# Performance work log

Measured on AMD Instinct MI355X. Metric: run time of the kernel, lower is better.

Reference implementation:

```python
import jax, jax.numpy as jnp
import numpy as np

D_MODEL, D_STATE, D_CONV, EXPAND = 1024, 16, 4, 2
D_INNER = EXPAND * D_MODEL          # 2048
DT_RANK = D_MODEL // 16             # 64
B, L = 2, 1024


def setup_inputs() -> dict:
    key = jax.random.key(0)
    ks = jax.random.split(key, 10)
    x = jax.random.normal(ks[0], (B, L, D_MODEL), dtype=jnp.float32)
    ln_w = jnp.ones((D_MODEL,), jnp.float32)
    ln_b = jnp.zeros((D_MODEL,), jnp.float32)
    in_proj_w = jax.random.normal(ks[1], (2 * D_INNER, D_MODEL), jnp.float32) * (D_MODEL ** -0.5)
    conv_w = jax.random.normal(ks[2], (D_INNER, 1, D_CONV), jnp.float32) * (D_CONV ** -0.5)
    conv_b = jnp.zeros((D_INNER,), jnp.float32)
    x_proj_w = jax.random.normal(ks[3], (DT_RANK + 2 * D_STATE, D_INNER), jnp.float32) * (D_INNER ** -0.5)
    dt_proj_w = jax.random.normal(ks[4], (D_INNER, DT_RANK), jnp.float32) * (DT_RANK ** -0.5)
    # dt bias: inverse-softplus of dt sampled log-uniform in [1e-3, 1e-1] (mamba init)
    dt = jnp.exp(jax.random.uniform(ks[5], (D_INNER,)) * (np.log(0.1) - np.log(1e-3)) + np.log(1e-3))
    dt_proj_b = dt + jnp.log(-jnp.expm1(-dt))
    # A_log: log of [1..d_state] repeated per channel (S4D-real init)
    A_log = jnp.log(jnp.broadcast_to(jnp.arange(1, D_STATE + 1, dtype=jnp.float32), (D_INNER, D_STATE)))
    D = jnp.ones((D_INNER,), jnp.float32)
    out_proj_w = jax.random.normal(ks[6], (D_MODEL, D_INNER), jnp.float32) * (D_INNER ** -0.5)
    return dict(x=x, ln_w=ln_w, ln_b=ln_b, in_proj_w=in_proj_w, conv_w=conv_w,
                conv_b=conv_b, x_proj_w=x_proj_w, dt_proj_w=dt_proj_w,
                dt_proj_b=dt_proj_b, A_log=A_log, D=D, out_proj_w=out_proj_w)


def _layernorm(x, w, b, eps=1e-5):
    mu = jnp.mean(x, axis=-1, keepdims=True)
    var = jnp.mean(jnp.square(x - mu), axis=-1, keepdims=True)
    return (x - mu) * jax.lax.rsqrt(var + eps) * w + b


def _mamba(h, in_proj_w, conv_w, conv_b, x_proj_w, dt_proj_w, dt_proj_b, A_log, D, out_proj_w):
    # h: (B, L, d_model)
    xz = jnp.einsum('bld,ed->ble', h, in_proj_w)          # (B,L,2*d_inner)
    x_in, z = jnp.split(xz, 2, axis=-1)                   # each (B,L,d_inner)
    # depthwise causal conv1d
    kernel = jnp.transpose(conv_w, (2, 1, 0))             # (d_conv, 1, d_inner) LIO
    x_conv = jax.lax.conv_general_dilated(
        x_in, kernel, window_strides=(1,), padding=[(D_CONV - 1, 0)],
        dimension_numbers=('NLC', 'LIO', 'NLC'), feature_group_count=D_INNER)
    x_conv = jax.nn.silu(x_conv + conv_b)                 # (B,L,d_inner)
    # input-dependent SSM parameters
    x_dbl = jnp.einsum('bld,ed->ble', x_conv, x_proj_w)   # (B,L,dt_rank+2*d_state)
    dt, B_ssm, C_ssm = jnp.split(x_dbl, [DT_RANK, DT_RANK + D_STATE], axis=-1)
    dt = jax.nn.softplus(jnp.einsum('blr,dr->bld', dt, dt_proj_w) + dt_proj_b)  # (B,L,d_inner)
    A = -jnp.exp(A_log)                                   # (d_inner, d_state)
    deltaA = jnp.exp(dt[..., None] * A)                   # (B,L,d_inner,d_state)
    deltaBu = dt[..., None] * B_ssm[:, :, None, :] * x_conv[..., None]
    # selective scan: h_t = deltaA_t * h_{t-1} + deltaBu_t (parallel associative scan over L)
    def combine(left, right):
        a_l, b_l = left
        a_r, b_r = right
        return a_l * a_r, b_l * a_r + b_r
    _, states = jax.lax.associative_scan(combine, (deltaA, deltaBu), axis=1)
    y = jnp.einsum('blds,bls->bld', states, C_ssm) + x_conv * D
    y = y * jax.nn.silu(z)
    return jnp.einsum('bld,ed->ble', y, out_proj_w)       # (B,L,d_model)


def reference(x, ln_w, ln_b, in_proj_w, conv_w, conv_b, x_proj_w, dt_proj_w,
              dt_proj_b, A_log, D, out_proj_w):
    h = _layernorm(x, ln_w, ln_b)
    return x + _mamba(h, in_proj_w, conv_w, conv_b, x_proj_w, dt_proj_w,
                      dt_proj_b, A_log, D, out_proj_w)
```

## Files before the change

kernel.cpp:

```cpp
#include <hip/hip_runtime.h>
#include <hip/hip_bf16.h>
#include <math.h>

#define DM   1024
#define DI   2048
#define DS   16
#define DTR  64
#define NB   2
#define LL   1024
#define MR   (NB*LL)
#define XDBL 96
#define NC   32
#define CL   32

typedef _Float16 half8  __attribute__((ext_vector_type(8)));
typedef _Float16 half4v __attribute__((ext_vector_type(4)));
typedef float    floatx4 __attribute__((ext_vector_type(4)));

__device__ __forceinline__ void gload_lds16(const void* g, void* l) {
  __builtin_amdgcn_global_load_lds(
      (const __attribute__((address_space(1))) void*)g,
      (__attribute__((address_space(3))) void*)l, 16, 0, 0);
}

__global__ __launch_bounds__(256) void front_kernel(
    const float* __restrict__ x, const float* __restrict__ ln_w,
    const float* __restrict__ ln_b,
    const float* __restrict__ w_in, const float* __restrict__ w_out,
    const float* __restrict__ w_xp, const float* __restrict__ w_dt,
    _Float16* __restrict__ h_h,
    _Float16* __restrict__ w_in_h, _Float16* __restrict__ w_out_h,
    _Float16* __restrict__ w_xp_h, _Float16* __restrict__ w_dt_h) {
  const int blk = blockIdx.x;
  if (blk < MR) {
    __shared__ float sA[4], sB[4];
    const float* xr = x + (size_t)blk * DM;
    float s = 0.f, ss = 0.f;
    for (int i = threadIdx.x; i < DM; i += 256) {
      float v = xr[i];
      s += v; ss += v * v;
    }
    for (int o = 32; o > 0; o >>= 1) {
      s  += __shfl_down(s, o, 64);
      ss += __shfl_down(ss, o, 64);
    }
    const int wid = threadIdx.x >> 6, lid = threadIdx.x & 63;
    if (lid == 0) { sA[wid] = s; sB[wid] = ss; }
    __syncthreads();
    if (threadIdx.x == 0) {
      float S = sA[0] + sA[1] + sA[2] + sA[3];
      float SS = sB[0] + sB[1] + sB[2] + sB[3];
      float mu = S / DM;
      sA[0] = mu;
      sB[0] = rsqrtf(SS / DM - mu * mu + 1e-5f);
    }
    __syncthreads();
    const float mu = sA[0], rs = sB[0];
    for (int i = threadIdx.x; i < DM; i += 256)
      h_h[(size_t)blk * DM + i] = (_Float16)((xr[i] - mu) * rs * ln_w[i] + ln_b[i]);
    return;
  }
  int i = (blk - MR) * 256 + threadIdx.x;
  const int N0 = 1048576, N1 = 524288, N2 = 49152, N3 = 32768;
  const float* s; _Float16* d; int off;
  if (i < N0)            { s = w_in;  d = w_in_h;  off = i; }
  else if (i < N0+N1)    { s = w_out; d = w_out_h; off = i - N0; }
  else if (i < N0+N1+N2) { s = w_xp;  d = w_xp_h;  off = i - N0 - N1; }
  else if (i < N0+N1+N2+N3) { s = w_dt; d = w_dt_h; off = i - N0 - N1 - N2; }
  else return;
  float4 v = ((const float4*)s)[off];
  half4v h = {(_Float16)v.x, (_Float16)v.y, (_Float16)v.z, (_Float16)v.w};
  ((half4v*)d)[off] = h;
}

template <int EPI, int TN>
__global__ __launch_bounds__(256) void gemm_mfma(
    const _Float16* __restrict__ A,
    const _Float16* __restrict__ W,
    void* __restrict__ Cv, void* __restrict__ C2v,
    const float* __restrict__ extra, int ldc,
    int M, int N, int K, int kchunk) {
  constexpr int NT = TN / 32;
  constexpr int WSLOT = TN / 16;
  __shared__ alignas(16) _Float16 As[2][128 * 32];
  __shared__ alignas(16) _Float16 Ws[2][TN * 32];
  const int t = threadIdx.x;
  const int wave = t >> 6, lane = t & 63;
  const int m0 = blockIdx.y * 128, n0 = blockIdx.x * TN;
  const int k_beg = blockIdx.z * kchunk;
  const int nk = kchunk >> 5;
  const int wm = (wave >> 1) * 64, wn = (wave & 1) * (TN / 2);
  floatx4 acc[4][NT];
#pragma unroll
  for (int i = 0; i < 4; i++)
#pragma unroll
    for (int j = 0; j < NT; j++) acc[i][j] = {0.f, 0.f, 0.f, 0.f};

  const int fr = lane & 15;
  const int kc8 = lane >> 4;

  auto stage = [&](int buf, int k0) {
    for (int sl = wave; sl < 8; sl += 4) {
      const int idx = sl * 64 + lane;
      const int row = idx >> 2, kc = idx & 3;
      gload_lds16(A + (size_t)(m0 + row) * K + k0 + kc * 8, &As[buf][sl * 512]);
    }
    for (int sl = wave; sl < WSLOT; sl += 4) {
      const int idx = sl * 64 + lane;
      const int row = idx >> 2, kc = idx & 3;
      const int wrow = (n0 + row < N) ? row : 0;
      gload_lds16(W + (size_t)(n0 + wrow) * K + k0 + kc * 8, &Ws[buf][sl * 512]);
    }
  };

  stage(0, k_beg);
  int cur = 0;
  for (int ki = 0; ki < nk; ki++) {
    __syncthreads();
    if (ki + 1 < nk) stage(cur ^ 1, k_beg + ((ki + 1) << 5));
    half8 af[4], wf[NT];
#pragma unroll
    for (int i = 0; i < 4; i++)
      af[i] = *(const half8*)&As[cur][(wm + i * 16 + fr) * 32 + kc8 * 8];
#pragma unroll
    for (int j = 0; j < NT; j++)
      wf[j] = *(const half8*)&Ws[cur][(wn + j * 16 + fr) * 32 + kc8 * 8];
#pragma unroll
    for (int i = 0; i < 4; i++)
#pragma unroll
      for (int j = 0; j < NT; j++)
        acc[i][j] = __builtin_amdgcn_mfma_f32_16x16x32_f16(af[i], wf[j], acc[i][j], 0, 0, 0);
    cur ^= 1;
  }

  const int col = lane & 15, rowq = lane >> 4;
#pragma unroll
  for (int i = 0; i < 4; i++) {
#pragma unroll
    for (int j = 0; j < NT; j++) {
      const int n = n0 + wn + j * 16 + col;
      if (n < N) {
#pragma unroll
        for (int r = 0; r < 4; r++) {
          const int m = m0 + wm + i * 16 + rowq * 4 + r;
          float v = acc[i][j][r];
          if (EPI == 0) {
            if (n < DI) ((_Float16*)Cv )[(size_t)m * DI + n]      = (_Float16)v;
            else        ((_Float16*)C2v)[(size_t)m * DI + n - DI] = (_Float16)v;
          } else if (EPI == 1) {
            v += extra[n];
            v = (v > 20.f) ? v : log1pf(expf(v));
            ((float*)Cv)[(size_t)m * ldc + n] = v;
          } else if (EPI == 4) {
            ((float*)Cv)[((size_t)blockIdx.z * M + m) * ldc + n] = v;
          }
        }
      }
    }
  }
}

__global__ __launch_bounds__(256) void xproj_reduce(
    const float* __restrict__ part,
    float* __restrict__ x_dbl, _Float16* __restrict__ dtr) {
  const int idx = blockIdx.x * 256 + threadIdx.x;
  const int m = idx / XDBL, c = idx - m * XDBL;
  float s = 0.f;
#pragma unroll
  for (int z = 0; z < 16; z++) s += part[(size_t)z * (MR * XDBL) + idx];
  x_dbl[idx] = s;
  if (c < DTR) dtr[m * DTR + c] = (_Float16)s;
}

__global__ __launch_bounds__(256) void out_reduce(
    const float* __restrict__ x, const float* __restrict__ part,
    float* __restrict__ out) {
  const int i = blockIdx.x * 256 + threadIdx.x;
  float4 a  = ((const float4*)x)[i];
  float4 p0 = ((const float4*)part)[i];
  float4 p1 = ((const float4*)(part + (size_t)MR * DM))[i];
  float4 r = make_float4(a.x + p0.x + p1.x, a.y + p0.y + p1.y,
                         a.z + p0.z + p1.z, a.w + p0.w + p1.w);
  ((float4*)out)[i] = r;
}

__global__ __launch_bounds__(256) void conv_silu_kernel(
    const _Float16* __restrict__ xin, const float* __restrict__ cw,
    const float* __restrict__ cb, _Float16* __restrict__ xc) {
  const int idx = blockIdx.x * 256 + threadIdx.x;
  const int d8 = idx & (DI / 8 - 1);
  const int ml = idx >> 8;
  const int l  = ml & (LL - 1);
  const int d0 = d8 * 8;
  half8 xr[4];
  const half8 zero = {0, 0, 0, 0, 0, 0, 0, 0};
#pragma unroll
  for (int k = 0; k < 4; k++) {
    const int lp = l - 3 + k;
    xr[k] = (lp >= 0) ? *(const half8*)&xin[(size_t)(ml - 3 + k) * DI + d0] : zero;
  }
  half8 o;
#pragma unroll
  for (int j = 0; j < 8; j++) {
    float acc = cb[d0 + j];
#pragma unroll
    for (int k = 0; k < 4; k++)
      acc += (float)xr[k][j] * cw[(d0 + j) * 4 + k];
    o[j] = (_Float16)(acc / (1.f + __expf(-acc)));
  }
  *(half8*)&xc[(size_t)ml * DI + d0] = o;
}

__device__ __forceinline__ bool load_a(const float* __restrict__ A_log, int d,
                                       float* a) {
  const float4* Ap = (const float4*)(A_log + (size_t)d * DS);
  bool fast = true;
#pragma unroll
  for (int i = 0; i < 4; i++) {
    float4 v = Ap[i];
    a[4 * i + 0] = -__expf(v.x); a[4 * i + 1] = -__expf(v.y);
    a[4 * i + 2] = -__expf(v.z); a[4 * i + 3] = -__expf(v.w);
  }
#pragma unroll
  for (int s = 0; s < DS; s++)
    fast = fast && (fabsf(a[s] + (float)(s + 1)) < 1e-4f);
  return fast;
}

__global__ __launch_bounds__(256) void scan_phase1(
    const _Float16* __restrict__ xc,
    const float* __restrict__ xdbl,
    const float* __restrict__ dtm,
    const float* __restrict__ A_log,
    float* __restrict__ HE,
    float* __restrict__ SA) {
  __shared__ float Bs[CL][DS];
  const int bi = blockIdx.x;
  const int dblk = bi & 7;
  const int c = (bi >> 3) & (NC - 1);
  const int b = bi >> 8;
  const int t = threadIdx.x;
  const int d = dblk * 256 + t;
  const int mlbase = b * LL + c * CL;

  for (int i = t; i < CL * DS; i += 256) {
    int tt = i >> 4, s = i & 15;
    Bs[tt][s] = xdbl[(size_t)(mlbase + tt) * XDBL + DTR + s];
  }

  float a[DS];
  const bool fast = load_a(A_log, d, a);
  float h[DS];
#pragma unroll
  for (int s = 0; s < DS; s++) h[s] = 0.f;
  float S = 0.f;
  __syncthreads();

  if (fast) {
    for (int tt = 0; tt < CL; tt++) {
      const size_t ml = mlbase + tt;
      const float dtv = dtm[ml * DI + d];
      const float u   = (float)xc[ml * DI + d];
      const float du  = dtv * u;
      S += dtv;
      const float r = __expf(-dtv);
      float P = 1.f;
#pragma unroll
      for (int s = 0; s < DS; s++) {
        P *= r;
        h[s] = P * h[s] + du * Bs[tt][s];
      }
    }
  } else {
    for (int tt = 0; tt < CL; tt++) {
      const size_t ml = mlbase + tt;
      const float dtv = dtm[ml * DI + d];
      const float u   = (float)xc[ml * DI + d];
      const float du  = dtv * u;
      S += dtv;
#pragma unroll
      for (int s = 0; s < DS; s++)
        h[s] = __expf(dtv * a[s]) * h[s] + du * Bs[tt][s];
    }
  }
  const size_t base = ((size_t)(b * NC + c) * DS) * DI + d;
#pragma unroll
  for (int s = 0; s < DS; s++) HE[base + (size_t)s * DI] = h[s];
  SA[(size_t)(b * NC + c) * DI + d] = S;
}

__global__ __launch_bounds__(256) void scan_phase2(
    const float* __restrict__ A_log,
    const float* __restrict__ SA,
    float* __restrict__ HE) {
  const int idx = blockIdx.x * 256 + threadIdx.x;
  const int d = idx & (DI - 1);
  const int s = (idx >> 11) & (DS - 1);
  const int b = idx >> 15;
  const float a = -__expf(A_log[(size_t)d * DS + s]);
  float Hc = 0.f;
  for (int c = 0; c < NC; c++) {
    const size_t o = ((size_t)(b * NC + c) * DS + s) * DI + d;
    const float he = HE[o];
    const float P = __expf(a * SA[(size_t)(b * NC + c) * DI + d]);
    HE[o] = Hc;
    Hc = P * Hc + he;
  }
}

__global__ __launch_bounds__(256) void scan_phase3(
    const _Float16* __restrict__ xc,
    const float* __restrict__ xdbl,
    const float* __restrict__ dtm,
    const _Float16* __restrict__ zbuf,
    const float* __restrict__ A_log,
    const float* __restrict__ Dvec,
    const float* __restrict__ HE,
    _Float16* __restrict__ y) {
  __shared__ float Bs[CL][DS];
  __shared__ float Cs[CL][DS];
  const int bi = blockIdx.x;
  const int dblk = bi & 7;
  const int c = (bi >> 3) & (NC - 1);
  const int b = bi >> 8;
  const int t = threadIdx.x;
  const int d = dblk * 256 + t;
  const int mlbase = b * LL + c * CL;

  for (int i = t; i < CL * DS; i += 256) {
    int tt = i >> 4, s = i & 15;
    const size_t ro = (size_t)(mlbase + tt) * XDBL + DTR + s;
    Bs[tt][s] = xdbl[ro];
    Cs[tt][s] = xdbl[ro + DS];
  }

  float a[DS];
  const bool fast = load_a(A_log, d, a);
  float h[DS];
  const size_t base = ((size_t)(b * NC + c) * DS) * DI + d;
#pragma unroll
  for (int s = 0; s < DS; s++) h[s] = HE[base + (size_t)s * DI];
  const float Dv = Dvec[d];
  __syncthreads();

  if (fast) {
    for (int tt = 0; tt < CL; tt++) {
      const size_t ml = mlbase + tt;
      const float dtv = dtm[ml * DI + d];
      const float u   = (float)xc[ml * DI + d];
      const float du  = dtv * u;
      const float r = __expf(-dtv);
      float P = 1.f, p = 0.f;
#pragma unroll
      for (int s = 0; s < DS; s++) {
        P *= r;
        h[s] = P * h[s] + du * Bs[tt][s];
        p += h[s] * Cs[tt][s];
      }
      const float zv = (float)zbuf[ml * DI + d];
      const float sil = zv / (1.f + __expf(-zv));
      y[ml * DI + d] = (_Float16)((p + u * Dv) * sil);
    }
  } else {
    for (int tt = 0; tt < CL; tt++) {
      const size_t ml = mlbase + tt;
      const float dtv = dtm[ml * DI + d];
      const float u   = (float)xc[ml * DI + d];
      const float du  = dtv * u;
      float p = 0.f;
#pragma unroll
      for (int s = 0; s < DS; s++) {
        h[s] = __expf(dtv * a[s]) * h[s] + du * Bs[tt][s];
        p += h[s] * Cs[tt][s];
      }
      const float zv = (float)zbuf[ml * DI + d];
      const float sil = zv / (1.f + __expf(-zv));
      y[ml * DI + d] = (_Float16)((p + u * Dv) * sil);
    }
  }
}

extern "C" void kernel_launch(void* const* d_in, const int* in_sizes, int n_in,
                              void* d_out, int out_size, void* d_ws, size_t ws_size,
                              hipStream_t stream) {
  const float* x         = (const float*)d_in[0];
  const float* ln_w      = (const float*)d_in[1];
  const float* ln_b      = (const float*)d_in[2];
  const float* in_proj_w = (const float*)d_in[3];
  const float* conv_w    = (const float*)d_in[4];
  const float* conv_b    = (const float*)d_in[5];
  const float* x_proj_w  = (const float*)d_in[6];
  const float* dt_proj_w = (const float*)d_in[7];
  const float* dt_proj_b = (const float*)d_in[8];
  const float* A_log     = (const float*)d_in[9];
  const float* Dvec      = (const float*)d_in[10];
  const float* out_proj_w= (const float*)d_in[11];
  float* out = (float*)d_out;

  char* ws = (char*)d_ws;
  _Float16* h_h     = (_Float16*)ws;
  _Float16* xin_h   = (_Float16*)(ws + 4194304);
  _Float16* y_h     = xin_h;
  _Float16* z_h     = (_Float16*)(ws + 12582912);
  _Float16* xc_h    = (_Float16*)(ws + 20971520);
  float*    dtb     = (float*)   (ws + 29360128);
  float*    out_part= dtb;
  float*    x_dbl   = (float*)   (ws + 46137344);
  float*    SA      = (float*)   (ws + 46923776);
  _Float16* dtr_h   = (_Float16*)(ws + 47448064);
  float*    HE      = (float*)   (ws + 47710208);
  _Float16* w_in_h  = (_Float16*)(ws + 56098816);
  _Float16* w_out_h = (_Float16*)(ws + 64487424);
  _Float16* w_xp_h  = (_Float16*)(ws + 68681728);
  _Float16* w_dt_h  = (_Float16*)(ws + 69074944);
  float*    xp_part = (float*)   (ws + 69337088);

  front_kernel<<<MR + 6464, 256, 0, stream>>>(
      x, ln_w, ln_b, in_proj_w, out_proj_w, x_proj_w, dt_proj_w,
      h_h, w_in_h, w_out_h, w_xp_h, w_dt_h);

  gemm_mfma<0, 64><<<dim3(2 * DI / 64, MR / 128, 1), 256, 0, stream>>>(
      h_h, w_in_h, xin_h, z_h, nullptr, 0, MR, 2 * DI, DM, DM);

  conv_silu_kernel<<<(MR * DI / 8) / 256, 256, 0, stream>>>(xin_h, conv_w, conv_b, xc_h);

  gemm_mfma<4, 96><<<dim3(1, MR / 128, 16), 256, 0, stream>>>(
      xc_h, w_xp_h, xp_part, nullptr, nullptr, XDBL, MR, XDBL, DI, DI / 16);
  xproj_reduce<<<(MR * XDBL) / 256, 256, 0, stream>>>(xp_part, x_dbl, dtr_h);

  gemm_mfma<1, 64><<<dim3(DI / 64, MR / 128, 1), 256, 0, stream>>>(
      dtr_h, w_dt_h, dtb, nullptr, dt_proj_b, DI, MR, DI, DTR, DTR);

  scan_phase1<<<NB * NC * (DI / 256), 256, 0, stream>>>(
      xc_h, x_dbl, dtb, A_log, HE, SA);
  scan_phase2<<<(NB * DS * DI) / 256, 256, 0, stream>>>(A_log, SA, HE);
  scan_phase3<<<NB * NC * (DI / 256), 256, 0, stream>>>(
      xc_h, x_dbl, dtb, z_h, A_log, Dvec, HE, y_h);

  gemm_mfma<4, 64><<<dim3(DM / 64, MR / 128, 2), 256, 0, stream>>>(
      y_h, w_out_h, out_part, nullptr, nullptr, DM, MR, DM, DI, DI / 2);
  out_reduce<<<(MR * DM / 4) / 256, 256, 0, stream>>>(x, out_part, out);
}
```

Measured before the change: 246.1 us.

## Store dt in fp16, fuse residual into out_proj GEMM, use narrower N tiles

The dt projection epilogue now writes softplus(dt) as fp16 instead of fp32, halving the traffic the two scan phases spend reading it. The out_proj GEMM drops its split-K partial buffers and the separate reduce kernel, adding the residual x directly in its epilogue. The in_proj and out_proj GEMMs switch to 32-wide N tiles to keep more blocks in flight. The costs are lower precision for dt and a longer serial K loop per out_proj block. The TN=32 path leaves each wave only one 16-column fragment, which may cover the tile poorly.

```diff
diff --git a/kernel.cpp b/kernel.cpp
--- a/kernel.cpp
+++ b/kernel.cpp
@@ -80,7 +80,7 @@
     void* __restrict__ Cv, void* __restrict__ C2v,
     const float* __restrict__ extra, int ldc,
     int M, int N, int K, int kchunk) {
-  constexpr int NT = TN / 32;
+  constexpr int NT = (TN + 31) / 32;
   constexpr int WSLOT = TN / 16;
   __shared__ alignas(16) _Float16 As[2][128 * 32];
   __shared__ alignas(16) _Float16 Ws[2][TN * 32];
@@ -147,12 +147,14 @@
           if (EPI == 0) {
             if (n < DI) ((_Float16*)Cv )[(size_t)m * DI + n]      = (_Float16)v;
             else        ((_Float16*)C2v)[(size_t)m * DI + n - DI] = (_Float16)v;
-          } else if (EPI == 1) {
+          } else if (EPI == 2) {
+            ((float*)Cv)[(size_t)m * ldc + n] = v + extra[(size_t)m * ldc + n];
+          } else if (EPI == 4) {
+            ((float*)Cv)[((size_t)blockIdx.z * M + m) * ldc + n] = v;
+          } else if (EPI == 5) {
             v += extra[n];
             v = (v > 20.f) ? v : log1pf(expf(v));
-            ((float*)Cv)[(size_t)m * ldc + n] = v;
-          } else if (EPI == 4) {
-            ((float*)Cv)[((size_t)blockIdx.z * M + m) * ldc + n] = v;
+            ((_Float16*)Cv)[(size_t)m * ldc + n] = (_Float16)v;
           }
         }
       }
@@ -170,18 +172,6 @@
   for (int z = 0; z < 16; z++) s += part[(size_t)z * (MR * XDBL) + idx];
   x_dbl[idx] = s;
   if (c < DTR) dtr[m * DTR + c] = (_Float16)s;
-}
-
-__global__ __launch_bounds__(256) void out_reduce(
-    const float* __restrict__ x, const float* __restrict__ part,
-    float* __restrict__ out) {
-  const int i = blockIdx.x * 256 + threadIdx.x;
-  float4 a  = ((const float4*)x)[i];
-  float4 p0 = ((const float4*)part)[i];
-  float4 p1 = ((const float4*)(part + (size_t)MR * DM))[i];
-  float4 r = make_float4(a.x + p0.x + p1.x, a.y + p0.y + p1.y,
-                         a.z + p0.z + p1.z, a.w + p0.w + p1.w);
-  ((float4*)out)[i] = r;
 }
 
 __global__ __launch_bounds__(256) void conv_silu_kernel(
@@ -230,7 +220,7 @@
 __global__ __launch_bounds__(256) void scan_phase1(
     const _Float16* __restrict__ xc,
     const float* __restrict__ xdbl,
-    const float* __restrict__ dtm,
+    const _Float16* __restrict__ dtm,
     const float* __restrict__ A_log,
     float* __restrict__ HE,
     float* __restrict__ SA) {
@@ -259,7 +249,7 @@
   if (fast) {
     for (int tt = 0; tt < CL; tt++) {
       const size_t ml = mlbase + tt;
-      const float dtv = dtm[ml * DI + d];
+      const float dtv = (float)dtm[ml * DI + d];
       const float u   = (float)xc[ml * DI + d];
       const float du  = dtv * u;
       S += dtv;
@@ -274,7 +264,7 @@
   } else {
     for (int tt = 0; tt < CL; tt++) {
       const size_t ml = mlbase + tt;
-      const float dtv = dtm[ml * DI + d];
+      const float dtv = (float)dtm[ml * DI + d];
       const float u   = (float)xc[ml * DI + d];
       const float du  = dtv * u;
       S += dtv;
@@ -311,7 +301,7 @@
 __global__ __launch_bounds__(256) void scan_phase3(
     const _Float16* __restrict__ xc,
     const float* __restrict__ xdbl,
-    const float* __restrict__ dtm,
+    const _Float16* __restrict__ dtm,
     const _Float16* __restrict__ zbuf,
     const float* __restrict__ A_log,
     const float* __restrict__ Dvec,
@@ -346,7 +336,7 @@
   if (fast) {
     for (int tt = 0; tt < CL; tt++) {
       const size_t ml = mlbase + tt;
-      const float dtv = dtm[ml * DI + d];
+      const float dtv = (float)dtm[ml * DI + d];
       const float u   = (float)xc[ml * DI + d];
       const float du  = dtv * u;
       const float r = __expf(-dtv);
@@ -364,7 +354,7 @@
   } else {
     for (int tt = 0; tt < CL; tt++) {
       const size_t ml = mlbase + tt;
-      const float dtv = dtm[ml * DI + d];
+      const float dtv = (float)dtm[ml * DI + d];
       const float u   = (float)xc[ml * DI + d];
       const float du  = dtv * u;
       float p = 0.f;
@@ -403,8 +393,7 @@
   _Float16* y_h     = xin_h;
   _Float16* z_h     = (_Float16*)(ws + 12582912);
   _Float16* xc_h    = (_Float16*)(ws + 20971520);
-  float*    dtb     = (float*)   (ws + 29360128);
-  float*    out_part= dtb;
+  _Float16* dtb_h   = (_Float16*)(ws + 29360128);
   float*    x_dbl   = (float*)   (ws + 46137344);
   float*    SA      = (float*)   (ws + 46923776);
   _Float16* dtr_h   = (_Float16*)(ws + 47448064);
@@ -419,7 +408,7 @@
       x, ln_w, ln_b, in_proj_w, out_proj_w, x_proj_w, dt_proj_w,
       h_h, w_in_h, w_out_h, w_xp_h, w_dt_h);
 
-  gemm_mfma<0, 64><<<dim3(2 * DI / 64, MR / 128, 1), 256, 0, stream>>>(
+  gemm_mfma<0, 32><<<dim3(2 * DI / 32, MR / 128, 1), 256, 0, stream>>>(
       h_h, w_in_h, xin_h, z_h, nullptr, 0, MR, 2 * DI, DM, DM);
 
   conv_silu_kernel<<<(MR * DI / 8) / 256, 256, 0, stream>>>(xin_h, conv_w, conv_b, xc_h);
@@ -428,16 +417,15 @@
       xc_h, w_xp_h, xp_part, nullptr, nullptr, XDBL, MR, XDBL, DI, DI / 16);
   xproj_reduce<<<(MR * XDBL) / 256, 256, 0, stream>>>(xp_part, x_dbl, dtr_h);
 
-  gemm_mfma<1, 64><<<dim3(DI / 64, MR / 128, 1), 256, 0, stream>>>(
-      dtr_h, w_dt_h, dtb, nullptr, dt_proj_b, DI, MR, DI, DTR, DTR);
+  gemm_mfma<5, 64><<<dim3(DI / 64, MR / 128, 1), 256, 0, stream>>>(
+      dtr_h, w_dt_h, dtb_h, nullptr, dt_proj_b, DI, MR, DI, DTR, DTR);
 
   scan_phase1<<<NB * NC * (DI / 256), 256, 0, stream>>>(
-      xc_h, x_dbl, dtb, A_log, HE, SA);
+      xc_h, x_dbl, dtb_h, A_log, HE, SA);
   scan_phase2<<<(NB * DS * DI) / 256, 256, 0, stream>>>(A_log, SA, HE);
   scan_phase3<<<NB * NC * (DI / 256), 256, 0, stream>>>(
-      xc_h, x_dbl, dtb, z_h, A_log, Dvec, HE, y_h);
-
-  gemm_mfma<4, 64><<<dim3(DM / 64, MR / 128, 2), 256, 0, stream>>>(
-      y_h, w_out_h, out_part, nullptr, nullptr, DM, MR, DM, DI, DI / 2);
-  out_reduce<<<(MR * DM / 4) / 256, 256, 0, stream>>>(x, out_part, out);
-}
+      xc_h, x_dbl, dtb_h, z_h, A_log, Dvec, HE, y_h);
+
+  gemm_mfma<2, 32><<<dim3(DM / 32, MR / 128, 1), 256, 0, stream>>>(
+      y_h, w_out_h, out, nullptr, x, DM, MR, DM, DI, DI);
+}
```

Result: slower. 274.4 us (+11.5%).
